# Kernel optimization log

Measured on AMD Instinct MI355X. Metric: run time of the kernel, lower is better.

Reference implementation:

```python
import jax, jax.numpy as jnp
import numpy as np
from jax import lax

HEADS = 8
LN_EPS = 1e-5


def setup_inputs() -> dict:
    key = jax.random.key(0)
    k = jax.random.split(key, 8)
    B, C, H, W, r = 4, 64, 64, 64, 4
    T = H * W
    x = jax.random.normal(k[0], (B, C, H, W), dtype=jnp.float32)
    conv_w = jax.random.normal(k[1], (C, C, r, r), dtype=jnp.float32) * 0.02  # OIHW
    conv_b = jnp.zeros((C,), dtype=jnp.float32)
    ln_g = jnp.ones((C,), dtype=jnp.float32)
    ln_b = jnp.zeros((C,), dtype=jnp.float32)
    Wqkv = jax.random.normal(k[2], (C, 3 * C), dtype=jnp.float32) * 0.02  # to_qvk (no bias)
    W0 = jax.random.normal(k[3], (C, C), dtype=jnp.float32) * 0.02  # output proj (no bias)
    E = jax.random.normal(k[4], (T, T // 4), dtype=jnp.float32)  # Linformer proj (randn in torch fwd)
    return {"x": x, "conv_w": conv_w, "conv_b": conv_b, "ln_g": ln_g,
            "ln_b": ln_b, "Wqkv": Wqkv, "W0": W0, "E": E}


def _layernorm2d(y, g, b):
    # LayerNorm over channel dim of NCHW (torch: permute to NHWC, LN last dim)
    yt = y.transpose(0, 2, 3, 1)  # b h w c
    mu = yt.mean(-1, keepdims=True)
    var = ((yt - mu) ** 2).mean(-1, keepdims=True)
    yt = (yt - mu) * lax.rsqrt(var + LN_EPS) * g + b
    return yt.transpose(0, 3, 1, 2)


def reference(x, conv_w, conv_b, ln_g, ln_b, Wqkv, W0, E):
    B, C, H, W = x.shape
    T = H * W
    dh = C // HEADS
    r = conv_w.shape[-1]

    # reducer: conv(stride=r) + LayerNorm2d. NOTE: faithful to the torch module,
    # this result is computed but NEVER used by the output (dead code in source).
    red = lax.conv_general_dilated(x, conv_w, (r, r), 'VALID',
                                   dimension_numbers=('NCHW', 'OIHW', 'NCHW'))
    red = red + conv_b[None, :, None, None]
    _red = _layernorm2d(red, ln_g, ln_b)  # unused, matches source

    # tokens from full-resolution x: b c h w -> b (h w) c
    xf = x.reshape(B, C, T).transpose(0, 2, 1)  # [B,T,C]
    qkv = xf @ Wqkv  # [B,T,3C]
    # rearrange 'b t (d k h)' with k=3, h=HEADS -> composite order (d, k, h)
    qkv = qkv.reshape(B, T, dh, 3, HEADS)
    q = qkv[:, :, :, 0, :].transpose(0, 3, 1, 2)  # [B,h,T,d]
    kk = qkv[:, :, :, 1, :].transpose(0, 3, 1, 2)
    v = qkv[:, :, :, 2, :].transpose(0, 3, 1, 2)

    # Linformer low-rank projection of V and K: [B,h,T,d] x [T,k] -> [B,h,k,d]
    v = jnp.einsum('bhjd,jk->bhkd', v, E)
    kk = jnp.einsum('bhjd,jk->bhkd', kk, E)

    scale = dh ** -0.5
    scores = jnp.einsum('bhid,bhjd->bhij', q, kk) * scale  # [B,h,T,k]
    attn = jax.nn.softmax(scores, axis=-1)
    out = jnp.einsum('bhij,bhjd->bhid', attn, v)  # [B,h,T,d]

    out = out.transpose(0, 2, 1, 3).reshape(B, T, C)  # b h i d -> b i (h d)
    out = out @ W0  # [B,T,C]
    return out.transpose(0, 2, 1).reshape(B, C, H, W)
```

## Files before the change

kernel.cpp:

```cpp
#include <hip/hip_runtime.h>

#define T_DIM 4096
#define KD    1024
#define SCALE 0.35355339059327373f
#define SCALE2 (0.35355339059327373f * 1.4426950408889634f)

extern "C" __device__ float __ocml_native_exp2_f32(float);

typedef __attribute__((ext_vector_type(8))) short bf16x8;
typedef __attribute__((ext_vector_type(4))) short bf16x4;
typedef __attribute__((ext_vector_type(4))) float f32x4;

__device__ inline unsigned short f2bf(float f) {
  unsigned u = __float_as_uint(f);
  unsigned r = u + 0x7fffu + ((u >> 16) & 1u);
  return (unsigned short)(r >> 16);
}

__device__ inline unsigned cvt_pk_bf16(float a, float b) {
  unsigned ua = __float_as_uint(a); ua += 0x7fffu + ((ua >> 16) & 1u);
  unsigned ub = __float_as_uint(b); ub += 0x7fffu + ((ub >> 16) & 1u);
  return (ua >> 16) | (ub & 0xffff0000u);
}

__device__ inline unsigned pk_trunc(float a, float b) {
  return (__float_as_uint(a) >> 16) | (__float_as_uint(b) & 0xffff0000u);
}

__device__ inline bf16x4 mk4(unsigned lo, unsigned hi) {
  union { unsigned u[2]; bf16x4 v; } x; x.u[0] = lo; x.u[1] = hi; return x.v;
}

__device__ inline bf16x8 mk8(unsigned a, unsigned b, unsigned c, unsigned d) {
  union { unsigned u[4]; bf16x8 v; } x;
  x.u[0] = a; x.u[1] = b; x.u[2] = c; x.u[3] = d; return x.v;
}

__device__ inline f32x4 mfma16(bf16x4 a, bf16x4 b, f32x4 c) {
  bf16x8 a8 = {}, b8 = {};
  a8[0] = a[0]; a8[1] = a[1]; a8[2] = a[2]; a8[3] = a[3];
  b8[0] = b[0]; b8[1] = b[1]; b8[2] = b[2]; b8[3] = b[3];
  return __builtin_amdgcn_mfma_f32_16x16x32_bf16(a8, b8, c, 0, 0, 0);
}

__global__ __launch_bounds__(256) void k_front(const float* __restrict__ x,
                                               const float* __restrict__ E,
                                               const float* __restrict__ Wqkv,
                                               float* __restrict__ partial,
                                               float* __restrict__ Q,
                                               float* __restrict__ out) {
  const int bid = blockIdx.x;
  const int tid = threadIdx.x;

  ((float4*)out)[(size_t)bid * 256 + tid] = make_float4(0.f, 0.f, 0.f, 0.f);

  if (bid < 512) {
    const int kb = bid & 7;
    const int b  = (bid >> 3) & 3;
    const int s  = bid >> 5;
    const int k0 = kb * 128;
    const int lane = tid & 63;
    const int w = tid >> 6;
    const int li = lane & 15, lg = lane >> 4;

    f32x4 acc[4][2] = {};
#pragma unroll 2
    for (int tb = 0; tb < 8; ++tb) {
      const int tbase = s * 256 + tb * 32 + lg * 8;
      bf16x8 bq[2];
#pragma unroll
      for (int nt = 0; nt < 2; ++nt) {
        const int kcol = k0 + w * 32 + nt * 16 + li;
        float bv[8];
#pragma unroll
        for (int j = 0; j < 8; ++j)
          bv[j] = E[(size_t)(tbase + j) * KD + kcol];
        bq[nt] = mk8(cvt_pk_bf16(bv[0], bv[1]), cvt_pk_bf16(bv[2], bv[3]),
                     cvt_pk_bf16(bv[4], bv[5]), cvt_pk_bf16(bv[6], bv[7]));
      }
#pragma unroll
      for (int mt = 0; mt < 4; ++mt) {
        const float* ap = x + ((size_t)b * 64 + mt * 16 + li) * T_DIM + tbase;
        float4 a0 = *(const float4*)(ap);
        float4 a1 = *(const float4*)(ap + 4);
        bf16x8 af8 = mk8(cvt_pk_bf16(a0.x, a0.y), cvt_pk_bf16(a0.z, a0.w),
                         cvt_pk_bf16(a1.x, a1.y), cvt_pk_bf16(a1.z, a1.w));
        acc[mt][0] = __builtin_amdgcn_mfma_f32_16x16x32_bf16(af8, bq[0], acc[mt][0], 0, 0, 0);
        acc[mt][1] = __builtin_amdgcn_mfma_f32_16x16x32_bf16(af8, bq[1], acc[mt][1], 0, 0, 0);
      }
    }
    float* pb = partial + ((size_t)s * 4 + b) * (64 * KD);
#pragma unroll
    for (int mt = 0; mt < 4; ++mt)
#pragma unroll
      for (int nt = 0; nt < 2; ++nt) {
        const int row = mt * 16 + lg * 4;
        const int col = k0 + w * 32 + nt * 16 + li;
#pragma unroll
        for (int reg = 0; reg < 4; ++reg)
          pb[(size_t)(row + reg) * KD + col] = acc[mt][nt][reg];
      }
  } else {
    const int idx = bid - 512;
    const int g  = idx & 7;
    const int tt = (idx >> 3) & 15;
    const int b  = idx >> 7;
    const int t  = tt * 256 + tid;
    const int col0 = g * 24;

    float acc[8];
#pragma unroll
    for (int j = 0; j < 8; ++j) acc[j] = 0.f;
    const float* xb = x + (size_t)b * 64 * T_DIM + t;
#pragma unroll 4
    for (int c = 0; c < 64; ++c) {
      float xv = xb[(size_t)c * T_DIM];
      const float* wr = Wqkv + c * 192 + col0;
#pragma unroll
      for (int h = 0; h < 8; ++h) acc[h] += xv * wr[h];
    }
#pragma unroll
    for (int h = 0; h < 8; ++h)
      Q[(((size_t)(b * 8 + h)) * 8 + g) * T_DIM + t] = acc[h];
  }
}

__global__ __launch_bounds__(256) void k_red(const float* __restrict__ partial,
                                             float* __restrict__ XPf) {
  const int gid = blockIdx.x * 256 + threadIdx.x;
  const int b  = gid >> 14;
  const int ck = gid & 16383;
  const float4* p4 = (const float4*)partial;
  float4 a = make_float4(0.f, 0.f, 0.f, 0.f);
#pragma unroll
  for (int s = 0; s < 16; ++s) {
    float4 v = p4[(size_t)(s * 4 + b) * 16384 + ck];
    a.x += v.x; a.y += v.y; a.z += v.z; a.w += v.w;
  }
  ((float4*)XPf)[gid] = a;
}

__global__ __launch_bounds__(256) void k_xkv(const float* __restrict__ XPf,
                                             const float* __restrict__ Wqkv,
                                             uint2* __restrict__ Kg,
                                             unsigned short* __restrict__ Vg) {
  const int kb = blockIdx.x;
  const int h  = blockIdx.y;
  const int b  = blockIdx.z;
  const int tid = threadIdx.x;

  const int klocal = tid & 63;
  const int sel    = (tid >> 6) & 1;
  const int dg     = tid >> 7;
  const int k      = kb * 64 + klocal;

  const float* xp = XPf + (size_t)b * 65536 + k;
  float acc[4];
#pragma unroll
  for (int d = 0; d < 4; ++d) acc[d] = 0.f;
#pragma unroll 8
  for (int c = 0; c < 64; ++c) {
    float xv = xp[(size_t)c * KD];
    const float* wr = Wqkv + c * 192 + (sel + 1) * 8 + h;
#pragma unroll
    for (int d = 0; d < 4; ++d) acc[d] += xv * wr[(dg * 4 + d) * 24];
  }

  const int bh = b * 8 + h;
  if (sel == 0) {
    uint2* kg = Kg + (size_t)bh * 2048;
    kg[dg * 1024 + k] = make_uint2(cvt_pk_bf16(acc[0] * SCALE2, acc[1] * SCALE2),
                                   cvt_pk_bf16(acc[2] * SCALE2, acc[3] * SCALE2));
  } else {
#pragma unroll
    for (int d = 0; d < 4; ++d)
      Vg[(size_t)(bh * 8 + dg * 4 + d) * KD + k] = f2bf(acc[d]);
  }
}

#define VT_PITCH 1032
__global__ __launch_bounds__(256) void k_attn(const float* __restrict__ Q,
                                              const uint2* __restrict__ Kg,
                                              const unsigned short* __restrict__ Vg,
                                              const float* __restrict__ W0,
                                              float* __restrict__ out) {
  __shared__ __attribute__((aligned(16))) unsigned short Kt[2 * 1024 * 4];
  __shared__ unsigned short Vt[9 * VT_PITCH];
  __shared__ float W0s[512];
  const int bh = blockIdx.x;
  const int tid = threadIdx.x;
  const int b = bh >> 3, h = bh & 7;

  const uint2* kg = Kg + (size_t)bh * 2048;
  uint2* kt2 = (uint2*)Kt;
#pragma unroll
  for (int it = 0; it < 8; ++it)
    kt2[it * 256 + tid] = kg[it * 256 + tid];
  const unsigned* vg = (const unsigned*)(Vg + (size_t)bh * 8192);
#pragma unroll
  for (int dd = 0; dd < 8; ++dd) {
#pragma unroll
    for (int it = 0; it < 2; ++it) {
      const int j2 = it * 256 + tid;
      *(unsigned*)(Vt + dd * VT_PITCH + j2 * 2) = vg[dd * 512 + j2];
    }
  }
#pragma unroll
  for (int it = 0; it < 2; ++it)
    *(unsigned*)(Vt + 8 * VT_PITCH + (it * 256 + tid) * 2) = 0x3F803F80u;
  W0s[tid]       = W0[h * 512 + tid];
  W0s[tid + 256] = W0[h * 512 + tid + 256];
  __syncthreads();

  const int lane = tid & 63, w = tid >> 6;
  const int li = lane & 15, lg = lane >> 4;
  const int i0w = blockIdx.y * 128 + w * 32;

  bf16x4 qf[2] = {bf16x4{}, bf16x4{}};
  if (lane < 32) {
#pragma unroll
    for (int it2 = 0; it2 < 2; ++it2) {
      const float* qp = Q + ((size_t)bh * 8 + lg * 4) * T_DIM + i0w + it2 * 16 + li;
      qf[it2] = mk4(cvt_pk_bf16(qp[0], qp[T_DIM]),
                    cvt_pk_bf16(qp[2 * T_DIM], qp[3 * T_DIM]));
    }
  }

  f32x4 accO[2] = {f32x4{0.f, 0.f, 0.f, 0.f}, f32x4{0.f, 0.f, 0.f, 0.f}};
#pragma unroll 2
  for (int jt = 0; jt < 1024; jt += 16) {
    bf16x4 kf = {};
    if (lane < 32) kf = *(const bf16x4*)(&Kt[(size_t)(lg * 1024 + jt + li) * 4]);
    bf16x4 vf = {};
    if (li < 9) vf = *(const bf16x4*)(&Vt[li * VT_PITCH + jt + lg * 4]);
#pragma unroll
    for (int it2 = 0; it2 < 2; ++it2) {
      f32x4 st = mfma16(kf, qf[it2], f32x4{0.f, 0.f, 0.f, 0.f});
      f32x4 p;
      p[0] = __ocml_native_exp2_f32(st[0]); p[1] = __ocml_native_exp2_f32(st[1]);
      p[2] = __ocml_native_exp2_f32(st[2]); p[3] = __ocml_native_exp2_f32(st[3]);
      bf16x4 pf = mk4(pk_trunc(p[0], p[1]), pk_trunc(p[2], p[3]));
      accO[it2] = mfma16(vf, pf, accO[it2]);
    }
  }

  __syncthreads();
  float* OwW = (float*)Kt + w * 256;

#pragma unroll
  for (int it2 = 0; it2 < 2; ++it2) {
    float l = __shfl(accO[it2][0], 32 + li);
    float inv = 1.0f / l;
    if (lane < 32) {
      float4 o = make_float4(accO[it2][0] * inv, accO[it2][1] * inv,
                             accO[it2][2] * inv, accO[it2][3] * inv);
      *(float4*)(OwW + (it2 * 16 + li) * 8 + lg * 4) = o;
    }
  }

  const int tok = lane & 31, ch = lane >> 5;
  float ov[8];
#pragma unroll
  for (int d = 0; d < 8; ++d) ov[d] = OwW[tok * 8 + d];
#pragma unroll 4
  for (int j = 0; j < 32; ++j) {
    const int c = ch * 32 + j;
    float a = 0.f;
#pragma unroll
    for (int d = 0; d < 8; ++d) a += ov[d] * W0s[d * 64 + c];
    atomicAdd(out + ((size_t)b * 64 + c) * T_DIM + i0w + tok, a);
  }
}

extern "C" void kernel_launch(void* const* d_in, const int* in_sizes, int n_in,
                              void* d_out, int out_size, void* d_ws, size_t ws_size,
                              hipStream_t stream) {
  const float* x    = (const float*)d_in[0];
  const float* Wqkv = (const float*)d_in[5];
  const float* W0   = (const float*)d_in[6];
  const float* E    = (const float*)d_in[7];
  float* out = (float*)d_out;

  float* Q           = (float*)d_ws;
  float* partial     = Q + 1048576;
  uint2* Kg          = (uint2*)(partial + 4194304);
  unsigned short* Vg = (unsigned short*)(Kg + 65536);
  float* XPf         = (float*)(Vg + 262144);

  k_front <<<dim3(1024),     256, 0, stream>>>(x, E, Wqkv, partial, Q, out);
  k_red   <<<dim3(256),      256, 0, stream>>>(partial, XPf);
  k_xkv   <<<dim3(16, 8, 4), 256, 0, stream>>>(XPf, Wqkv, Kg, Vg);
  k_attn  <<<dim3(32, 32),   256, 0, stream>>>(Q, Kg, Vg, W0, out);
}
```

Measured before the change: 149.0 us.

## Fuse four kernels into one persistent kernel with software grid barriers

Merges the front projection, partial reduction, K/V projection and attention kernels into a single 512-block kernel that separates phases with an atomic counter/generation grid barrier. Each block now does work from both branches of the old front kernel and handles two query tiles in attention, which reuses the K/V tiles staged in shared memory. The aim is to remove three kernel launch gaps and the tail idle time between them. In exchange it relies on all 512 blocks being co-resident (launch bounds of 256 threads, 2 blocks per unit), which risks deadlock if they are not. It also halves the grid for the attention phase and adds barrier spin overhead.

```diff
diff --git a/kernel.cpp b/kernel.cpp
--- a/kernel.cpp
+++ b/kernel.cpp
@@ -4,6 +4,8 @@
 #define KD    1024
 #define SCALE 0.35355339059327373f
 #define SCALE2 (0.35355339059327373f * 1.4426950408889634f)
+#define VT_PITCH 1032
+#define NBLK 512
 
 extern "C" __device__ float __ocml_native_exp2_f32(float);
 
@@ -43,18 +45,53 @@
   return __builtin_amdgcn_mfma_f32_16x16x32_bf16(a8, b8, c, 0, 0, 0);
 }
 
-__global__ __launch_bounds__(256) void k_front(const float* __restrict__ x,
-                                               const float* __restrict__ E,
-                                               const float* __restrict__ Wqkv,
-                                               float* __restrict__ partial,
-                                               float* __restrict__ Q,
-                                               float* __restrict__ out) {
+__device__ unsigned g_bar_cnt = 0;
+__device__ unsigned g_bar_gen = 0;
+
+__device__ inline void grid_sync_sw() {
+  __syncthreads();
+  if (threadIdx.x == 0) {
+    __threadfence();
+    unsigned gen = __hip_atomic_load(&g_bar_gen, __ATOMIC_RELAXED,
+                                     __HIP_MEMORY_SCOPE_AGENT);
+    unsigned arr = __hip_atomic_fetch_add(&g_bar_cnt, 1u, __ATOMIC_ACQ_REL,
+                                          __HIP_MEMORY_SCOPE_AGENT);
+    if (arr == NBLK - 1u) {
+      __hip_atomic_store(&g_bar_cnt, 0u, __ATOMIC_RELAXED,
+                         __HIP_MEMORY_SCOPE_AGENT);
+      __hip_atomic_store(&g_bar_gen, gen + 1u, __ATOMIC_RELEASE,
+                         __HIP_MEMORY_SCOPE_AGENT);
+    } else {
+      while (__hip_atomic_load(&g_bar_gen, __ATOMIC_ACQUIRE,
+                               __HIP_MEMORY_SCOPE_AGENT) == gen)
+        __builtin_amdgcn_s_sleep(2);
+    }
+  }
+  __syncthreads();
+  __threadfence();
+}
+
+__global__ __launch_bounds__(256, 2) void k_all(
+    const float* __restrict__ x, const float* __restrict__ E,
+    const float* __restrict__ Wqkv, const float* __restrict__ W0,
+    float* __restrict__ partial, float* __restrict__ Q,
+    uint2* __restrict__ Kg, unsigned short* __restrict__ Vg,
+    float* __restrict__ XPf, float* __restrict__ out)
+{
+  __shared__ __attribute__((aligned(16))) unsigned short Kt[2 * 1024 * 4];
+  __shared__ unsigned short Vt[9 * VT_PITCH];
+  __shared__ float W0s[512];
+
   const int bid = blockIdx.x;
   const int tid = threadIdx.x;
 
-  ((float4*)out)[(size_t)bid * 256 + tid] = make_float4(0.f, 0.f, 0.f, 0.f);
-
-  if (bid < 512) {
+  {
+    float4* o4 = (float4*)out;
+    o4[(size_t)bid * 512 + tid]       = make_float4(0.f, 0.f, 0.f, 0.f);
+    o4[(size_t)bid * 512 + tid + 256] = make_float4(0.f, 0.f, 0.f, 0.f);
+  }
+
+  {
     const int kb = bid & 7;
     const int b  = (bid >> 3) & 3;
     const int s  = bid >> 5;
@@ -100,11 +137,12 @@
         for (int reg = 0; reg < 4; ++reg)
           pb[(size_t)(row + reg) * KD + col] = acc[mt][nt][reg];
       }
-  } else {
-    const int idx = bid - 512;
-    const int g  = idx & 7;
-    const int tt = (idx >> 3) & 15;
-    const int b  = idx >> 7;
+  }
+
+  {
+    const int g  = bid & 7;
+    const int tt = (bid >> 3) & 15;
+    const int b  = bid >> 7;
     const int t  = tt * 256 + tid;
     const int col0 = g * 24;
 
@@ -123,152 +161,156 @@
     for (int h = 0; h < 8; ++h)
       Q[(((size_t)(b * 8 + h)) * 8 + g) * T_DIM + t] = acc[h];
   }
-}
-
-__global__ __launch_bounds__(256) void k_red(const float* __restrict__ partial,
-                                             float* __restrict__ XPf) {
-  const int gid = blockIdx.x * 256 + threadIdx.x;
-  const int b  = gid >> 14;
-  const int ck = gid & 16383;
-  const float4* p4 = (const float4*)partial;
-  float4 a = make_float4(0.f, 0.f, 0.f, 0.f);
-#pragma unroll
-  for (int s = 0; s < 16; ++s) {
-    float4 v = p4[(size_t)(s * 4 + b) * 16384 + ck];
-    a.x += v.x; a.y += v.y; a.z += v.z; a.w += v.w;
-  }
-  ((float4*)XPf)[gid] = a;
-}
-
-__global__ __launch_bounds__(256) void k_xkv(const float* __restrict__ XPf,
-                                             const float* __restrict__ Wqkv,
-                                             uint2* __restrict__ Kg,
-                                             unsigned short* __restrict__ Vg) {
-  const int kb = blockIdx.x;
-  const int h  = blockIdx.y;
-  const int b  = blockIdx.z;
-  const int tid = threadIdx.x;
-
-  const int klocal = tid & 63;
-  const int sel    = (tid >> 6) & 1;
-  const int dg     = tid >> 7;
-  const int k      = kb * 64 + klocal;
-
-  const float* xp = XPf + (size_t)b * 65536 + k;
-  float acc[4];
-#pragma unroll
-  for (int d = 0; d < 4; ++d) acc[d] = 0.f;
+
+  grid_sync_sw();
+
+  if (tid < 128) {
+    const int f4 = bid * 128 + tid;
+    const int b  = f4 >> 14;
+    const int ck = f4 & 16383;
+    const float4* p4 = (const float4*)partial;
+    float4 a = make_float4(0.f, 0.f, 0.f, 0.f);
+#pragma unroll
+    for (int s = 0; s < 16; ++s) {
+      float4 v = p4[(size_t)(s * 4 + b) * 16384 + ck];
+      a.x += v.x; a.y += v.y; a.z += v.z; a.w += v.w;
+    }
+    ((float4*)XPf)[f4] = a;
+  }
+
+  grid_sync_sw();
+
+  {
+    const int kb = bid & 15;
+    const int h  = (bid >> 4) & 7;
+    const int b  = bid >> 7;
+
+    const int klocal = tid & 63;
+    const int sel    = (tid >> 6) & 1;
+    const int dg     = tid >> 7;
+    const int k      = kb * 64 + klocal;
+
+    const float* xp = XPf + (size_t)b * 65536 + k;
+    float acc[4];
+#pragma unroll
+    for (int d = 0; d < 4; ++d) acc[d] = 0.f;
 #pragma unroll 8
-  for (int c = 0; c < 64; ++c) {
-    float xv = xp[(size_t)c * KD];
-    const float* wr = Wqkv + c * 192 + (sel + 1) * 8 + h;
-#pragma unroll
-    for (int d = 0; d < 4; ++d) acc[d] += xv * wr[(dg * 4 + d) * 24];
-  }
-
-  const int bh = b * 8 + h;
-  if (sel == 0) {
-    uint2* kg = Kg + (size_t)bh * 2048;
-    kg[dg * 1024 + k] = make_uint2(cvt_pk_bf16(acc[0] * SCALE2, acc[1] * SCALE2),
-                                   cvt_pk_bf16(acc[2] * SCALE2, acc[3] * SCALE2));
-  } else {
-#pragma unroll
-    for (int d = 0; d < 4; ++d)
-      Vg[(size_t)(bh * 8 + dg * 4 + d) * KD + k] = f2bf(acc[d]);
-  }
-}
-
-#define VT_PITCH 1032
-__global__ __launch_bounds__(256) void k_attn(const float* __restrict__ Q,
-                                              const uint2* __restrict__ Kg,
-                                              const unsigned short* __restrict__ Vg,
-                                              const float* __restrict__ W0,
-                                              float* __restrict__ out) {
-  __shared__ __attribute__((aligned(16))) unsigned short Kt[2 * 1024 * 4];
-  __shared__ unsigned short Vt[9 * VT_PITCH];
-  __shared__ float W0s[512];
-  const int bh = blockIdx.x;
-  const int tid = threadIdx.x;
-  const int b = bh >> 3, h = bh & 7;
-
-  const uint2* kg = Kg + (size_t)bh * 2048;
-  uint2* kt2 = (uint2*)Kt;
-#pragma unroll
-  for (int it = 0; it < 8; ++it)
-    kt2[it * 256 + tid] = kg[it * 256 + tid];
-  const unsigned* vg = (const unsigned*)(Vg + (size_t)bh * 8192);
-#pragma unroll
-  for (int dd = 0; dd < 8; ++dd) {
-#pragma unroll
-    for (int it = 0; it < 2; ++it) {
-      const int j2 = it * 256 + tid;
-      *(unsigned*)(Vt + dd * VT_PITCH + j2 * 2) = vg[dd * 512 + j2];
-    }
-  }
-#pragma unroll
-  for (int it = 0; it < 2; ++it)
-    *(unsigned*)(Vt + 8 * VT_PITCH + (it * 256 + tid) * 2) = 0x3F803F80u;
-  W0s[tid]       = W0[h * 512 + tid];
-  W0s[tid + 256] = W0[h * 512 + tid + 256];
-  __syncthreads();
-
-  const int lane = tid & 63, w = tid >> 6;
-  const int li = lane & 15, lg = lane >> 4;
-  const int i0w = blockIdx.y * 128 + w * 32;
-
-  bf16x4 qf[2] = {bf16x4{}, bf16x4{}};
-  if (lane < 32) {
-#pragma unroll
-    for (int it2 = 0; it2 < 2; ++it2) {
-      const float* qp = Q + ((size_t)bh * 8 + lg * 4) * T_DIM + i0w + it2 * 16 + li;
-      qf[it2] = mk4(cvt_pk_bf16(qp[0], qp[T_DIM]),
-                    cvt_pk_bf16(qp[2 * T_DIM], qp[3 * T_DIM]));
-    }
-  }
-
-  f32x4 accO[2] = {f32x4{0.f, 0.f, 0.f, 0.f}, f32x4{0.f, 0.f, 0.f, 0.f}};
+    for (int c = 0; c < 64; ++c) {
+      float xv = xp[(size_t)c * KD];
+      const float* wr = Wqkv + c * 192 + (sel + 1) * 8 + h;
+#pragma unroll
+      for (int d = 0; d < 4; ++d) acc[d] += xv * wr[(dg * 4 + d) * 24];
+    }
+
+    const int bh = b * 8 + h;
+    if (sel == 0) {
+      uint2* kg = Kg + (size_t)bh * 2048;
+      kg[dg * 1024 + k] = make_uint2(cvt_pk_bf16(acc[0] * SCALE2, acc[1] * SCALE2),
+                                     cvt_pk_bf16(acc[2] * SCALE2, acc[3] * SCALE2));
+    } else {
+#pragma unroll
+      for (int d = 0; d < 4; ++d)
+        Vg[(size_t)(bh * 8 + dg * 4 + d) * KD + k] = f2bf(acc[d]);
+    }
+  }
+
+  grid_sync_sw();
+
+  {
+    const int bh = bid & 31;
+    const int iy = bid >> 5;
+    const int b = bh >> 3, h = bh & 7;
+
+    const uint2* kg = Kg + (size_t)bh * 2048;
+    uint2* kt2 = (uint2*)Kt;
+#pragma unroll
+    for (int it = 0; it < 8; ++it)
+      kt2[it * 256 + tid] = kg[it * 256 + tid];
+    const unsigned* vg = (const unsigned*)(Vg + (size_t)bh * 8192);
+#pragma unroll
+    for (int dd = 0; dd < 8; ++dd) {
+#pragma unroll
+      for (int it = 0; it < 2; ++it) {
+        const int j2 = it * 256 + tid;
+        *(unsigned*)(Vt + dd * VT_PITCH + j2 * 2) = vg[dd * 512 + j2];
+      }
+    }
+#pragma unroll
+    for (int it = 0; it < 2; ++it)
+      *(unsigned*)(Vt + 8 * VT_PITCH + (it * 256 + tid) * 2) = 0x3F803F80u;
+    W0s[tid]       = W0[h * 512 + tid];
+    W0s[tid + 256] = W0[h * 512 + tid + 256];
+    __syncthreads();
+
+    const int lane = tid & 63, w = tid >> 6;
+    const int li = lane & 15, lg = lane >> 4;
+
+    bf16x4 qf[2][2];
+#pragma unroll
+    for (int tt = 0; tt < 2; ++tt) { qf[tt][0] = bf16x4{}; qf[tt][1] = bf16x4{}; }
+    if (lane < 32) {
+#pragma unroll
+      for (int tt = 0; tt < 2; ++tt) {
+        const int i0 = (iy + tt * 16) * 128 + w * 32;
+#pragma unroll
+        for (int it2 = 0; it2 < 2; ++it2) {
+          const float* qp = Q + ((size_t)bh * 8 + lg * 4) * T_DIM + i0 + it2 * 16 + li;
+          qf[tt][it2] = mk4(cvt_pk_bf16(qp[0], qp[T_DIM]),
+                            cvt_pk_bf16(qp[2 * T_DIM], qp[3 * T_DIM]));
+        }
+      }
+    }
+
+    f32x4 accO[2][2] = {};
 #pragma unroll 2
-  for (int jt = 0; jt < 1024; jt += 16) {
-    bf16x4 kf = {};
-    if (lane < 32) kf = *(const bf16x4*)(&Kt[(size_t)(lg * 1024 + jt + li) * 4]);
-    bf16x4 vf = {};
-    if (li < 9) vf = *(const bf16x4*)(&Vt[li * VT_PITCH + jt + lg * 4]);
-#pragma unroll
-    for (int it2 = 0; it2 < 2; ++it2) {
-      f32x4 st = mfma16(kf, qf[it2], f32x4{0.f, 0.f, 0.f, 0.f});
-      f32x4 p;
-      p[0] = __ocml_native_exp2_f32(st[0]); p[1] = __ocml_native_exp2_f32(st[1]);
-      p[2] = __ocml_native_exp2_f32(st[2]); p[3] = __ocml_native_exp2_f32(st[3]);
-      bf16x4 pf = mk4(pk_trunc(p[0], p[1]), pk_trunc(p[2], p[3]));
-      accO[it2] = mfma16(vf, pf, accO[it2]);
-    }
-  }
-
-  __syncthreads();
-  float* OwW = (float*)Kt + w * 256;
-
-#pragma unroll
-  for (int it2 = 0; it2 < 2; ++it2) {
-    float l = __shfl(accO[it2][0], 32 + li);
-    float inv = 1.0f / l;
-    if (lane < 32) {
-      float4 o = make_float4(accO[it2][0] * inv, accO[it2][1] * inv,
-                             accO[it2][2] * inv, accO[it2][3] * inv);
-      *(float4*)(OwW + (it2 * 16 + li) * 8 + lg * 4) = o;
-    }
-  }
-
-  const int tok = lane & 31, ch = lane >> 5;
-  float ov[8];
-#pragma unroll
-  for (int d = 0; d < 8; ++d) ov[d] = OwW[tok * 8 + d];
+    for (int jt = 0; jt < 1024; jt += 16) {
+      bf16x4 kf = {};
+      if (lane < 32) kf = *(const bf16x4*)(&Kt[(size_t)(lg * 1024 + jt + li) * 4]);
+      bf16x4 vf = {};
+      if (li < 9) vf = *(const bf16x4*)(&Vt[li * VT_PITCH + jt + lg * 4]);
+#pragma unroll
+      for (int tt = 0; tt < 2; ++tt)
+#pragma unroll
+        for (int it2 = 0; it2 < 2; ++it2) {
+          f32x4 st = mfma16(kf, qf[tt][it2], f32x4{0.f, 0.f, 0.f, 0.f});
+          f32x4 p;
+          p[0] = __ocml_native_exp2_f32(st[0]); p[1] = __ocml_native_exp2_f32(st[1]);
+          p[2] = __ocml_native_exp2_f32(st[2]); p[3] = __ocml_native_exp2_f32(st[3]);
+          bf16x4 pf = mk4(pk_trunc(p[0], p[1]), pk_trunc(p[2], p[3]));
+          accO[tt][it2] = mfma16(vf, pf, accO[tt][it2]);
+        }
+    }
+
+    __syncthreads();
+    float* OwW = (float*)Kt + w * 256;
+    const int tok = lane & 31, ch = lane >> 5;
+
+#pragma unroll
+    for (int tt = 0; tt < 2; ++tt) {
+      const int i0 = (iy + tt * 16) * 128 + w * 32;
+#pragma unroll
+      for (int it2 = 0; it2 < 2; ++it2) {
+        float l = __shfl(accO[tt][it2][0], 32 + li);
+        float inv = 1.0f / l;
+        if (lane < 32) {
+          float4 o = make_float4(accO[tt][it2][0] * inv, accO[tt][it2][1] * inv,
+                                 accO[tt][it2][2] * inv, accO[tt][it2][3] * inv);
+          *(float4*)(OwW + (it2 * 16 + li) * 8 + lg * 4) = o;
+        }
+      }
+
+      float ov[8];
+#pragma unroll
+      for (int d = 0; d < 8; ++d) ov[d] = OwW[tok * 8 + d];
 #pragma unroll 4
-  for (int j = 0; j < 32; ++j) {
-    const int c = ch * 32 + j;
-    float a = 0.f;
-#pragma unroll
-    for (int d = 0; d < 8; ++d) a += ov[d] * W0s[d * 64 + c];
-    atomicAdd(out + ((size_t)b * 64 + c) * T_DIM + i0w + tok, a);
+      for (int j = 0; j < 32; ++j) {
+        const int c = ch * 32 + j;
+        float a = 0.f;
+#pragma unroll
+        for (int d = 0; d < 8; ++d) a += ov[d] * W0s[d * 64 + c];
+        atomicAdd(out + ((size_t)b * 64 + c) * T_DIM + i0 + tok, a);
+      }
+    }
   }
 }
 
@@ -287,8 +329,6 @@
   unsigned short* Vg = (unsigned short*)(Kg + 65536);
   float* XPf         = (float*)(Vg + 262144);
 
-  k_front <<<dim3(1024),     256, 0, stream>>>(x, E, Wqkv, partial, Q, out);
-  k_red   <<<dim3(256),      256, 0, stream>>>(partial, XPf);
-  k_xkv   <<<dim3(16, 8, 4), 256, 0, stream>>>(XPf, Wqkv, Kg, Vg);
-  k_attn  <<<dim3(32, 32),   256, 0, stream>>>(Q, Kg, Vg, W0, out);
-}
+  k_all<<<dim3(NBLK), dim3(256), 0, stream>>>(x, E, Wqkv, W0,
+                                              partial, Q, Kg, Vg, XPf, out);
+}
```

New measurement: 481.0 us. 223% more time.
